# Performance work log

Hardware: AMD Instinct MI355X
Metric: run time of the kernel (lower is better)

## Reference

```python
import jax, jax.numpy as jnp
import numpy as np

DOMAIN_MIN, DOMAIN_MAX = -1.0, 1.0
N, D_IN, D_OUT, K = 1024, 128, 128, 8


def setup_inputs() -> dict:
    key = jax.random.key(0)
    k1, k2, k3 = jax.random.split(key, 3)
    x = jax.random.uniform(k1, (N, D_IN), dtype=jnp.float32,
                           minval=DOMAIN_MIN, maxval=DOMAIN_MAX)
    # Per-edge spline knot values: near-identity init plus small noise.
    base = jnp.linspace(DOMAIN_MIN, DOMAIN_MAX, K, dtype=jnp.float32)
    coeffs = base[None, None, :] + 0.1 * jax.random.normal(
        k2, (D_OUT, D_IN, K), dtype=jnp.float32)
    weights = jax.random.normal(k3, (D_OUT, D_IN), dtype=jnp.float32) * np.sqrt(2.0 / D_IN)
    bias = jnp.zeros((D_OUT,), dtype=jnp.float32)
    return {"x": x, "coeffs": coeffs, "weights": weights, "bias": bias}


def _spline_all_edges(x, coeffs):
    """Evaluate every edge's cubic (Catmull-Rom) spline at its input.
    x: [N, d_in]; coeffs: [d_out, d_in, K] knot values on uniform knots in [-1,1].
    Returns s: [N, d_in, d_out]."""
    K_ = coeffs.shape[-1]
    h = (DOMAIN_MAX - DOMAIN_MIN) / (K_ - 1)
    xc = jnp.clip(x, DOMAIN_MIN, DOMAIN_MAX)
    t = (xc - DOMAIN_MIN) / h                      # [N, d_in], in [0, K-1]
    idx = jnp.clip(jnp.floor(t).astype(jnp.int32), 0, K_ - 2)
    u = t - idx                                    # local coord in [0,1]
    i0 = jnp.clip(idx - 1, 0, K_ - 1)
    i1 = idx
    i2 = idx + 1
    i3 = jnp.clip(idx + 2, 0, K_ - 1)
    ct = jnp.transpose(coeffs, (1, 2, 0))          # [d_in, K, d_out]
    jar = jnp.arange(ct.shape[0])[None, :]          # [1, d_in]
    p0 = ct[jar, i0]                               # [N, d_in, d_out]
    p1 = ct[jar, i1]
    p2 = ct[jar, i2]
    p3 = ct[jar, i3]
    u2 = u * u
    u3 = u2 * u
    b0 = 0.5 * (-u3 + 2.0 * u2 - u)
    b1 = 0.5 * (3.0 * u3 - 5.0 * u2 + 2.0)
    b2 = 0.5 * (-3.0 * u3 + 4.0 * u2 + u)
    b3 = 0.5 * (u3 - u2)
    return (b0[..., None] * p0 + b1[..., None] * p1 +
            b2[..., None] * p2 + b3[..., None] * p3)


def reference(x, coeffs, weights, bias):
    # h_i(x) = sum_j w_ij * s_ij(x_j) + b_i
    s = _spline_all_edges(x, coeffs)               # [N, d_in, d_out]
    return jnp.einsum('njo,oj->no', s, weights) + bias[None, :]
```

## Files before the change

### kernel.cpp

```cpp
#include <hip/hip_runtime.h>
#include <hip/hip_bf16.h>
#include <stdint.h>


#define DIN 128
#define DOUT 128
#define KTOT 1024

typedef unsigned int u32;
typedef unsigned long long u64;
typedef unsigned short u16;
typedef __attribute__((ext_vector_type(8))) short bf16x8;
typedef __attribute__((ext_vector_type(4))) float f32x4;

union H8 { u16 s[8]; uint4 v; };

__device__ __forceinline__ u16 f2b(float f) {
    union { __hip_bfloat16 h; u16 u; } c;
    c.h = __float2bfloat16(f);
    return c.u;
}

__global__ __launch_bounds__(1024, 8) void kan_fused(
    const float* __restrict__ x, const float* __restrict__ coeffs,
    const float* __restrict__ weights, const float* __restrict__ bias,
    float* __restrict__ out)
{
    __shared__ __align__(16) u16 sBas[16 * KTOT];
    __shared__ __align__(16) u16 sWp [16 * KTOT];
    __shared__ __align__(16) float sC[16 * 256];

    const int tid  = threadIdx.x;
    const int wave = tid >> 6;
    const int lane = tid & 63;
    const int n0 = blockIdx.x * 16;
    const int o0 = blockIdx.y * 16;

    #pragma unroll
    for (int it = 0; it < 2; ++it) {
        const int task = tid + it * 1024;
        const int row = task >> 7;
        const int j = task & 127;
        float xv = x[n0 * DIN + task];
        xv = fminf(fmaxf(xv, -1.0f), 1.0f);
        const float t = (xv + 1.0f) * 3.5f;
        int idx = (int)t; idx = idx > 6 ? 6 : idx;
        const float u = t - (float)idx;
        const float u2 = u * u, u3 = u2 * u;
        const float b0 = 0.5f * (-u3 + 2.0f * u2 - u);
        const float b1 = 0.5f * (3.0f * u3 - 5.0f * u2 + 2.0f);
        const float b2 = 0.5f * (-3.0f * u3 + 4.0f * u2 + u);
        const float b3 = 0.5f * (u3 - u2);
        const bool e0 = (idx == 0), e6 = (idx == 6);
        const float m0 = e0 ? b0 + b1 : b0;
        const float m1 = e0 ? b2 : b1;
        const float m2 = e0 ? b3 : (e6 ? b2 + b3 : b2);
        const float m3 = e0 ? 0.0f : b3;
        const u32 lo32 = (u32)f2b(m0) | ((u32)f2b(m1) << 16);
        const u32 hi32 = (u32)f2b(m2) | ((u32)f2b(m3) << 16);
        const u64 q64 = ((u64)hi32 << 32) | lo32;
        const int sh = e0 ? 0 : (idx - 1) * 16;
        unsigned __int128 v = (unsigned __int128)q64 << sh;
        uint4 stv;
        stv.x = (u32)v;
        stv.y = (u32)(v >> 32);
        stv.z = (u32)(v >> 64);
        stv.w = (u32)(v >> 96);
        const int uu = j ^ (row & 7);
        *(uint4*)(sBas + row * KTOT + uu * 8) = stv;
    }

    #pragma unroll
    for (int it = 0; it < 2; ++it) {
        const int task = tid + it * 1024;
        const int o = task >> 7;
        const int j = task & 127;
        const float wv = weights[o0 * DIN + task];
        const float4 c0 = *(const float4*)(coeffs + o0 * KTOT + task * 8);
        const float4 c1 = *(const float4*)(coeffs + o0 * KTOT + task * 8 + 4);
        H8 h;
        h.s[0] = f2b(c0.x * wv); h.s[1] = f2b(c0.y * wv);
        h.s[2] = f2b(c0.z * wv); h.s[3] = f2b(c0.w * wv);
        h.s[4] = f2b(c1.x * wv); h.s[5] = f2b(c1.y * wv);
        h.s[6] = f2b(c1.z * wv); h.s[7] = f2b(c1.w * wv);
        const int uu = j ^ (o & 7);
        *(uint4*)(sWp + o * KTOT + uu * 8) = h.v;
    }
    __syncthreads();

    const int mo = lane & 15;
    const int q  = lane >> 4;
    const int sw = mo & 7;
    f32x4 acc = {0.0f, 0.0f, 0.0f, 0.0f};
    #pragma unroll
    for (int s = 0; s < 2; ++s) {
        const int S = wave * 2 + s;
        const int uu = (S * 4 + q) ^ sw;
        bf16x8 af = *(const bf16x8*)(sBas + mo * KTOT + uu * 8);
        bf16x8 bf = *(const bf16x8*)(sWp  + mo * KTOT + uu * 8);
        acc = __builtin_amdgcn_mfma_f32_16x16x32_bf16(af, bf, acc, 0, 0, 0);
    }

    #pragma unroll
    for (int r = 0; r < 4; ++r)
        sC[wave * 256 + (q * 4 + r) * 16 + mo] = acc[r];
    __syncthreads();

    if (tid < 256) {
        const int row = tid >> 4, col = tid & 15;
        float v = sC[tid];
        #pragma unroll
        for (int w = 1; w < 16; ++w) v += sC[w * 256 + tid];
        out[(n0 + row) * DOUT + o0 + col] = v + bias[o0 + col];
    }
}

extern "C" void kernel_launch(void* const* d_in, const int* in_sizes, int n_in,
                              void* d_out, int out_size, void* d_ws, size_t ws_size,
                              hipStream_t stream) {
    const float* x       = (const float*)d_in[0];
    const float* coeffs  = (const float*)d_in[1];
    const float* weights = (const float*)d_in[2];
    const float* bias    = (const float*)d_in[3];
    float* out = (float*)d_out;
    const int N = in_sizes[0] / DIN;
    dim3 grid(N / 16, DOUT / 16);
    kan_fused<<<grid, 1024, 0, stream>>>(x, coeffs, weights, bias, out);
}
```

Before: 61.40 us.

## Build MFMA operands directly in registers, dropping LDS staging and barrier

Each lane now computes its own spline-basis A fragment and weight-scaled coefficient B fragment straight from global memory into registers, then feeds them to the MFMA. The shared-memory staging buffers, their swizzled stores and loads, and the first __syncthreads are removed. The aim is to cut LDS traffic and a block-wide barrier. In exchange, global loads are less coalesced because each lane reads strided rows of x, weights and coeffs.

```diff
diff --git a/kernel.cpp b/kernel.cpp
--- a/kernel.cpp
+++ b/kernel.cpp
@@ -13,7 +13,7 @@
 typedef __attribute__((ext_vector_type(8))) short bf16x8;
 typedef __attribute__((ext_vector_type(4))) float f32x4;
 
-union H8 { u16 s[8]; uint4 v; };
+union H8 { u16 s[8]; uint4 v; bf16x8 b; };
 
 __device__ __forceinline__ u16 f2b(float f) {
     union { __hip_bfloat16 h; u16 u; } c;
@@ -26,8 +26,6 @@
     const float* __restrict__ weights, const float* __restrict__ bias,
     float* __restrict__ out)
 {
-    __shared__ __align__(16) u16 sBas[16 * KTOT];
-    __shared__ __align__(16) u16 sWp [16 * KTOT];
     __shared__ __align__(16) float sC[16 * 256];
 
     const int tid  = threadIdx.x;
@@ -36,12 +34,19 @@
     const int n0 = blockIdx.x * 16;
     const int o0 = blockIdx.y * 16;
 
+    const int mo = lane & 15;
+    const int q  = lane >> 4;
+
+    const float* xrow = x       + (size_t)(n0 + mo) * DIN;
+    const float* wrow = weights + (size_t)(o0 + mo) * DIN;
+    const float* crow = coeffs  + (size_t)(o0 + mo) * (DIN * 8);
+
+    f32x4 acc = {0.0f, 0.0f, 0.0f, 0.0f};
     #pragma unroll
-    for (int it = 0; it < 2; ++it) {
-        const int task = tid + it * 1024;
-        const int row = task >> 7;
-        const int j = task & 127;
-        float xv = x[n0 * DIN + task];
+    for (int s = 0; s < 2; ++s) {
+        const int j = wave * 8 + s * 4 + q;
+
+        float xv = xrow[j];
         xv = fminf(fmaxf(xv, -1.0f), 1.0f);
         const float t = (xv + 1.0f) * 3.5f;
         int idx = (int)t; idx = idx > 6 ? 6 : idx;
@@ -60,45 +65,23 @@
         const u32 hi32 = (u32)f2b(m2) | ((u32)f2b(m3) << 16);
         const u64 q64 = ((u64)hi32 << 32) | lo32;
         const int sh = e0 ? 0 : (idx - 1) * 16;
-        unsigned __int128 v = (unsigned __int128)q64 << sh;
-        uint4 stv;
-        stv.x = (u32)v;
-        stv.y = (u32)(v >> 32);
-        stv.z = (u32)(v >> 64);
-        stv.w = (u32)(v >> 96);
-        const int uu = j ^ (row & 7);
-        *(uint4*)(sBas + row * KTOT + uu * 8) = stv;
-    }
+        unsigned __int128 v128 = (unsigned __int128)q64 << sh;
+        H8 a;
+        a.v.x = (u32)v128;
+        a.v.y = (u32)(v128 >> 32);
+        a.v.z = (u32)(v128 >> 64);
+        a.v.w = (u32)(v128 >> 96);
 
-    #pragma unroll
-    for (int it = 0; it < 2; ++it) {
-        const int task = tid + it * 1024;
-        const int o = task >> 7;
-        const int j = task & 127;
-        const float wv = weights[o0 * DIN + task];
-        const float4 c0 = *(const float4*)(coeffs + o0 * KTOT + task * 8);
-        const float4 c1 = *(const float4*)(coeffs + o0 * KTOT + task * 8 + 4);
-        H8 h;
-        h.s[0] = f2b(c0.x * wv); h.s[1] = f2b(c0.y * wv);
-        h.s[2] = f2b(c0.z * wv); h.s[3] = f2b(c0.w * wv);
-        h.s[4] = f2b(c1.x * wv); h.s[5] = f2b(c1.y * wv);
-        h.s[6] = f2b(c1.z * wv); h.s[7] = f2b(c1.w * wv);
-        const int uu = j ^ (o & 7);
-        *(uint4*)(sWp + o * KTOT + uu * 8) = h.v;
-    }
-    __syncthreads();
+        const float wv = wrow[j];
+        const float4 c0 = *(const float4*)(crow + j * 8);
+        const float4 c1 = *(const float4*)(crow + j * 8 + 4);
+        H8 b;
+        b.s[0] = f2b(c0.x * wv); b.s[1] = f2b(c0.y * wv);
+        b.s[2] = f2b(c0.z * wv); b.s[3] = f2b(c0.w * wv);
+        b.s[4] = f2b(c1.x * wv); b.s[5] = f2b(c1.y * wv);
+        b.s[6] = f2b(c1.z * wv); b.s[7] = f2b(c1.w * wv);
 
-    const int mo = lane & 15;
-    const int q  = lane >> 4;
-    const int sw = mo & 7;
-    f32x4 acc = {0.0f, 0.0f, 0.0f, 0.0f};
-    #pragma unroll
-    for (int s = 0; s < 2; ++s) {
-        const int S = wave * 2 + s;
-        const int uu = (S * 4 + q) ^ sw;
-        bf16x8 af = *(const bf16x8*)(sBas + mo * KTOT + uu * 8);
-        bf16x8 bf = *(const bf16x8*)(sWp  + mo * KTOT + uu * 8);
-        acc = __builtin_amdgcn_mfma_f32_16x16x32_bf16(af, bf, acc, 0, 0, 0);
+        acc = __builtin_amdgcn_mfma_f32_16x16x32_bf16(a.b, b.b, acc, 0, 0, 0);
     }
 
     #pragma unroll
```

New measurement: 66.55 us. 1.08x slower.

## Widen output tile to 32 columns per block and prefetch global loads upfront

Applied to the files above, without the earlier changes.

Each workgroup now covers 16 rows by 32 output columns instead of 16 by 16. The grid is halved and flattened, so every basis tile built from x is reused by twice as many outputs. The 16 waves are split into two output tiles with 8 K-groups each, and the final reduction sums 8 partials instead of 16. All x, weights and coeffs loads are issued up front into registers so their latency overlaps. This raises register and shared-memory use (sWp doubles to 64 KB) and lowers the launch-bounds occupancy hint, leaving fewer blocks to spread across the GPU.

```diff
diff --git a/kernel.cpp b/kernel.cpp
--- a/kernel.cpp
+++ b/kernel.cpp
@@ -21,27 +21,41 @@
     return c.u;
 }
 
-__global__ __launch_bounds__(1024, 8) void kan_fused(
+__global__ __launch_bounds__(1024, 4) void kan_fused(
     const float* __restrict__ x, const float* __restrict__ coeffs,
     const float* __restrict__ weights, const float* __restrict__ bias,
     float* __restrict__ out)
 {
     __shared__ __align__(16) u16 sBas[16 * KTOT];
-    __shared__ __align__(16) u16 sWp [16 * KTOT];
+    __shared__ __align__(16) u16 sWp [32 * KTOT];
     __shared__ __align__(16) float sC[16 * 256];
 
     const int tid  = threadIdx.x;
     const int wave = tid >> 6;
     const int lane = tid & 63;
-    const int n0 = blockIdx.x * 16;
-    const int o0 = blockIdx.y * 16;
+    const int wg = blockIdx.x;
+    const int n0 = (wg >> 2) * 16;
+    const int o0 = (wg & 3) * 32;
+
+    float xv0, xv1;
+    float wv[4];
+    float4 ca[4], cb[4];
+    xv0 = x[n0 * DIN + tid];
+    xv1 = x[n0 * DIN + tid + 1024];
+    #pragma unroll
+    for (int it = 0; it < 4; ++it) {
+        const int task = tid + it * 1024;
+        wv[it] = weights[o0 * DIN + task];
+        ca[it] = *(const float4*)(coeffs + o0 * KTOT + task * 8);
+        cb[it] = *(const float4*)(coeffs + o0 * KTOT + task * 8 + 4);
+    }
 
     #pragma unroll
     for (int it = 0; it < 2; ++it) {
         const int task = tid + it * 1024;
         const int row = task >> 7;
         const int j = task & 127;
-        float xv = x[n0 * DIN + task];
+        float xv = it == 0 ? xv0 : xv1;
         xv = fminf(fmaxf(xv, -1.0f), 1.0f);
         const float t = (xv + 1.0f) * 3.5f;
         int idx = (int)t; idx = idx > 6 ? 6 : idx;
@@ -71,18 +85,18 @@
     }
 
     #pragma unroll
-    for (int it = 0; it < 2; ++it) {
+    for (int it = 0; it < 4; ++it) {
         const int task = tid + it * 1024;
         const int o = task >> 7;
         const int j = task & 127;
-        const float wv = weights[o0 * DIN + task];
-        const float4 c0 = *(const float4*)(coeffs + o0 * KTOT + task * 8);
-        const float4 c1 = *(const float4*)(coeffs + o0 * KTOT + task * 8 + 4);
+        const float w_ = wv[it];
+        const float4 c0 = ca[it];
+        const float4 c1 = cb[it];
         H8 h;
-        h.s[0] = f2b(c0.x * wv); h.s[1] = f2b(c0.y * wv);
-        h.s[2] = f2b(c0.z * wv); h.s[3] = f2b(c0.w * wv);
-        h.s[4] = f2b(c1.x * wv); h.s[5] = f2b(c1.y * wv);
-        h.s[6] = f2b(c1.z * wv); h.s[7] = f2b(c1.w * wv);
+        h.s[0] = f2b(c0.x * w_); h.s[1] = f2b(c0.y * w_);
+        h.s[2] = f2b(c0.z * w_); h.s[3] = f2b(c0.w * w_);
+        h.s[4] = f2b(c1.x * w_); h.s[5] = f2b(c1.y * w_);
+        h.s[6] = f2b(c1.z * w_); h.s[7] = f2b(c1.w * w_);
         const int uu = j ^ (o & 7);
         *(uint4*)(sWp + o * KTOT + uu * 8) = h.v;
     }
@@ -90,14 +104,17 @@
 
     const int mo = lane & 15;
     const int q  = lane >> 4;
+    const int ot = wave >> 3;
+    const int kg = wave & 7;
     const int sw = mo & 7;
+    const u16* bRow = sWp + (ot * 16 + mo) * KTOT;
     f32x4 acc = {0.0f, 0.0f, 0.0f, 0.0f};
     #pragma unroll
-    for (int s = 0; s < 2; ++s) {
-        const int S = wave * 2 + s;
+    for (int s = 0; s < 4; ++s) {
+        const int S = kg * 4 + s;
         const int uu = (S * 4 + q) ^ sw;
         bf16x8 af = *(const bf16x8*)(sBas + mo * KTOT + uu * 8);
-        bf16x8 bf = *(const bf16x8*)(sWp  + mo * KTOT + uu * 8);
+        bf16x8 bf = *(const bf16x8*)(bRow + uu * 8);
         acc = __builtin_amdgcn_mfma_f32_16x16x32_bf16(af, bf, acc, 0, 0, 0);
     }
 
@@ -106,12 +123,15 @@
         sC[wave * 256 + (q * 4 + r) * 16 + mo] = acc[r];
     __syncthreads();
 
-    if (tid < 256) {
-        const int row = tid >> 4, col = tid & 15;
-        float v = sC[tid];
+    if (tid < 512) {
+        const int ot2 = tid >> 8;
+        const int idx = tid & 255;
+        const int row = idx >> 4, col = idx & 15;
+        float v = sC[ot2 * 2048 + idx];
         #pragma unroll
-        for (int w = 1; w < 16; ++w) v += sC[w * 256 + tid];
-        out[(n0 + row) * DOUT + o0 + col] = v + bias[o0 + col];
+        for (int k = 1; k < 8; ++k) v += sC[ot2 * 2048 + k * 256 + idx];
+        const int oc = o0 + ot2 * 16 + col;
+        out[(n0 + row) * DOUT + oc] = v + bias[oc];
     }
 }
 
@@ -124,6 +144,6 @@
     const float* bias    = (const float*)d_in[3];
     float* out = (float*)d_out;
     const int N = in_sizes[0] / DIN;
-    dim3 grid(N / 16, DOUT / 16);
+    dim3 grid((N / 16) * (DOUT / 32));
     kan_fused<<<grid, 1024, 0, stream>>>(x, coeffs, weights, bias, out);
 }
```

After: 61.50 us. Within noise of the previous version (+0.2%).
